# Kernel optimization log

Hardware: AMD Instinct MI355X
Metric: run time of the kernel (lower is better)

Reference implementation:

```python
import jax, jax.numpy as jnp
import numpy as np


def _block(x, a, b):
    # [..., W, H, D] -> [..., W//a, H//b, a, b, D]
    w, h, d = x.shape[-3:]
    x = jnp.reshape(x, x.shape[:-3] + (w // a, a, h // b, b, d))
    return jnp.moveaxis(x, -4, -3)


def _combine(x, bs):
    # [..., W, H, D] -> [..., W//bs, H//bs, bs*bs*D]
    x = _block(x, bs, bs)
    return jnp.reshape(x, x.shape[:-3] + (-1,))


def _normalize(x):
    x = x - jnp.mean(x, axis=-1, keepdims=True)
    return x / (jnp.linalg.norm(x, axis=-1, keepdims=True) + 1e-05)


def setup_inputs() -> dict:
    key = jax.random.key(0)
    k1, k2 = jax.random.split(key)
    x = jax.random.normal(k1, (8, 128, 128, 64), dtype=jnp.float32)
    y = jax.random.normal(k2, (8, 128, 128, 64), dtype=jnp.float32)
    return {"x": x, "y": y, "blocksize": 4}


def reference(x, y, blocksize):
    shape = x.shape
    xc = _normalize(_combine(x, blocksize))  # [B, W/bs, H/bs, F]
    yc = _normalize(_combine(y, blocksize))
    yf = jnp.reshape(yc, (-1, yc.shape[-1]))  # [M, F] codebook
    # single similarity matrix, reused for min-loss and argmax (original
    # computed jnp.inner twice -- same math)
    sim = jnp.einsum('...f,mf->...m', xc, yf)  # [B, W/bs, H/bs, M]
    cosloss = jnp.mean(jnp.min(1.0 - sim, axis=-1))
    idx = jnp.argmax(sim, axis=-1)
    # one-hot matmul against yf == top-1 gather (argmax picks first max, as
    # does the original I = (argmax - arange == 0) construction)
    new_x = jnp.take(yf, idx, axis=0)  # [B, W/bs, H/bs, F]
    new_x = jnp.reshape(new_x, new_x.shape[:-1] + (blocksize, blocksize, -1))
    new_x = jnp.swapaxes(new_x, -4, -3)
    new_x = jnp.reshape(new_x, shape)
    return cosloss, new_x
```

## Files before the change

kernel.cpp:

```cpp
#include <hip/hip_runtime.h>
#include <math.h>


#define NROWS 8192
#define KY 1024
#define NCH 32
#define EPS 3e-4f
#define FEPS 8e-4f

typedef _Float16 v8h __attribute__((ext_vector_type(8)));
typedef float f32x4 __attribute__((ext_vector_type(4)));

__device__ __forceinline__ void gload16(const _Float16* g, _Float16* l) {
    __builtin_amdgcn_global_load_lds(
        (const __attribute__((address_space(1))) void*)g,
        (__attribute__((address_space(3))) void*)l, 16, 0, 0);
}

__device__ __forceinline__ unsigned umax(unsigned a, unsigned b) { return a > b ? a : b; }
__device__ __forceinline__ unsigned umin(unsigned a, unsigned b) { return a < b ? a : b; }

__device__ __forceinline__ unsigned packKey(float v, int col) {
    unsigned b = __float_as_uint(v);
    b ^= (unsigned)((int)b >> 31) | 0x80000000u;
    return (b & 0xFFFFE000u) | (unsigned)(8191 - col);
}

__device__ __forceinline__ float unpackApprox(unsigned k) {
    unsigned kb = k & 0xFFFFE000u;
    unsigned b = (kb & 0x80000000u) ? (kb ^ 0x80000000u) : ~kb;
    return __uint_as_float(b);
}

#define KMERGE(a1, a2, a3, b1, b2, b3) do {                                 \
    unsigned _n1 = umax(a1, b1);                                            \
    unsigned _n2 = umax(umin(a1, b1), umax(a2, b2));                        \
    unsigned _n3 = umax(umax(a3, b3), umax(umin(a1, b2), umin(a2, b1)));    \
    a1 = _n1; a2 = _n2; a3 = _n3;                                           \
} while (0)

__global__ __launch_bounds__(256) void normSplitKernel(
    const float* __restrict__ x, const float* __restrict__ y,
    _Float16* __restrict__ Xh, _Float16* __restrict__ Xl,
    _Float16* __restrict__ Yh, _Float16* __restrict__ Yl,
    int* __restrict__ flagCnt) {
    if (blockIdx.x == 0 && threadIdx.x == 0) *flagCnt = 0;
    int gr = blockIdx.x * 4 + (threadIdx.x >> 6);
    int ln = threadIdx.x & 63;
    bool isX = gr < NROWS;
    int row = isX ? gr : gr - NROWS;
    const float* src = isX ? x : y;
    _Float16* dh = isX ? Xh : Yh;
    _Float16* dl = isX ? Xl : Yl;
    int b = row >> 10, wq = (row >> 5) & 31, hq = row & 31;
    int a = ln >> 4, c = (ln >> 2) & 3, d0 = (ln & 3) << 4;
    const float* p = &src[(((size_t)(b * 128) + wq * 4 + a) * 128 + hq * 4 + c) * 64 + d0];
    float vv[16];
    *(float4*)(vv + 0)  = *(const float4*)(p + 0);
    *(float4*)(vv + 4)  = *(const float4*)(p + 4);
    *(float4*)(vv + 8)  = *(const float4*)(p + 8);
    *(float4*)(vv + 12) = *(const float4*)(p + 12);
    double s = 0.0;
    #pragma unroll
    for (int q = 0; q < 16; q++) s += (double)vv[q];
    #pragma unroll
    for (int m = 1; m < 64; m <<= 1) s += __shfl_xor(s, m, 64);
    double mean = s * (1.0 / 1024.0);
    double ss = 0.0;
    #pragma unroll
    for (int q = 0; q < 16; q++) {
        double d = (double)vv[q] - mean;
        ss += d * d;
    }
    #pragma unroll
    for (int m = 1; m < 64; m <<= 1) ss += __shfl_xor(ss, m, 64);
    double scale = 1.0 / (sqrt(ss) + 1e-5);
    _Float16 hi[16], lo[16];
    #pragma unroll
    for (int q = 0; q < 16; q++) {
        float f = (float)(((double)vv[q] - mean) * scale);
        _Float16 h = (_Float16)f;
        hi[q] = h;
        lo[q] = (_Float16)(f - (float)h);
    }
    size_t f0 = (size_t)row * KY + (ln << 4);
    *(v8h*)&dh[f0]     = *(v8h*)(hi);
    *(v8h*)&dh[f0 + 8] = *(v8h*)(hi + 8);
    *(v8h*)&dl[f0]     = *(v8h*)(lo);
    *(v8h*)&dl[f0 + 8] = *(v8h*)(lo + 8);
}

__global__ __launch_bounds__(512, 2) void simKernel(
    const _Float16* __restrict__ Xh, const _Float16* __restrict__ Yh,
    float* __restrict__ pV1, unsigned* __restrict__ pK1,
    unsigned* __restrict__ pK2, unsigned* __restrict__ pK3) {
    __shared__ __align__(16) _Float16 As[2][2][128 * 64];
    __shared__ __align__(16) _Float16 Bs[2][2][128 * 64];
    __shared__ unsigned sK[2][4][128][3];
    __shared__ float sE[2][4][128];
    const int t = threadIdx.x;
    const int l = t & 63, w = t >> 6;
    const int wr = w >> 2, wc = w & 3;
    const int quad = l >> 4, lm = l & 15;
    const int flat = blockIdx.x;
    const int bx = flat >> 5, by = flat & 31;
    const int r0 = bx * 256, c0 = by * 256;

    f32x4 acc[8][4];
    #pragma unroll
    for (int i = 0; i < 8; i++)
        #pragma unroll
        for (int j = 0; j < 4; j++) acc[i][j] = (f32x4){0.f, 0.f, 0.f, 0.f};

    const int lh = l >> 3;
    const int scol = ((l & 7) ^ lh) << 3;
    const _Float16* gA = Xh + (size_t)(r0 + w * 8 + lh) * KY + scol;
    const _Float16* gB = Yh + (size_t)(c0 + w * 8 + lh) * KY + scol;
    const int w512 = w * 512;

#define STAGE_H(Ms, gM, bb, h, ktt) do {                                       \
    gload16(gM + (size_t)((h) * 128) * KY + (ktt) * 64,      &Ms[bb][h][w512]); \
    gload16(gM + (size_t)((h) * 128 + 64) * KY + (ktt) * 64, &Ms[bb][h][w512 + 4096]); \
} while (0)

    const int sw7 = lm & 7;
    const int cK0 = (quad ^ sw7) << 3;
    const int cK1 = ((4 + quad) ^ sw7) << 3;
    const int aOff = lm * 64;
    const int bSub = (wc & 1) * 4096 + lm * 64;

    STAGE_H(As, gA, 0, 0, 0); STAGE_H(As, gA, 0, 1, 0);
    STAGE_H(Bs, gB, 0, 0, 0); STAGE_H(Bs, gB, 0, 1, 0);
    asm volatile("s_waitcnt vmcnt(0)" ::: "memory");
    __builtin_amdgcn_s_barrier();

    #pragma unroll 1
    for (int kt = 0; kt < 16; kt++) {
        const int b = kt & 1, bn = b ^ 1;
        const int ktn = (kt + 1) & 15;
        const _Float16* Ah = &As[b][wr][0];
        const _Float16* Bh = &Bs[b][wc >> 1][0];
        v8h af[4], bf[4];

        #pragma unroll
        for (int i = 0; i < 4; i++) af[i] = *(const v8h*)&Ah[i * 1024 + aOff + cK0];
        #pragma unroll
        for (int j = 0; j < 4; j++) bf[j] = *(const v8h*)&Bh[bSub + j * 1024 + cK0];
        STAGE_H(As, gA, bn, 0, ktn);
        __builtin_amdgcn_s_barrier();
        asm volatile("s_waitcnt lgkmcnt(0)" ::: "memory");
        __builtin_amdgcn_sched_barrier(0);
        __builtin_amdgcn_s_setprio(1);
        #pragma unroll
        for (int j = 0; j < 4; j++)
            #pragma unroll
            for (int i = 0; i < 4; i++)
                acc[i][j] = __builtin_amdgcn_mfma_f32_16x16x32_f16(af[i], bf[j], acc[i][j], 0, 0, 0);
        __builtin_amdgcn_s_setprio(0);
        __builtin_amdgcn_s_barrier();

        #pragma unroll
        for (int i = 0; i < 4; i++) af[i] = *(const v8h*)&Ah[4096 + i * 1024 + aOff + cK0];
        STAGE_H(As, gA, bn, 1, ktn);
        __builtin_amdgcn_s_barrier();
        asm volatile("s_waitcnt lgkmcnt(0)" ::: "memory");
        __builtin_amdgcn_sched_barrier(0);
        __builtin_amdgcn_s_setprio(1);
        #pragma unroll
        for (int j = 0; j < 4; j++)
            #pragma unroll
            for (int i = 0; i < 4; i++)
                acc[4 + i][j] = __builtin_amdgcn_mfma_f32_16x16x32_f16(af[i], bf[j], acc[4 + i][j], 0, 0, 0);
        __builtin_amdgcn_s_setprio(0);
        __builtin_amdgcn_s_barrier();

        #pragma unroll
        for (int i = 0; i < 4; i++) af[i] = *(const v8h*)&Ah[i * 1024 + aOff + cK1];
        #pragma unroll
        for (int j = 0; j < 4; j++) bf[j] = *(const v8h*)&Bh[bSub + j * 1024 + cK1];
        STAGE_H(Bs, gB, bn, 0, ktn);
        __builtin_amdgcn_s_barrier();
        asm volatile("s_waitcnt lgkmcnt(0)" ::: "memory");
        __builtin_amdgcn_sched_barrier(0);
        __builtin_amdgcn_s_setprio(1);
        #pragma unroll
        for (int j = 0; j < 4; j++)
            #pragma unroll
            for (int i = 0; i < 4; i++)
                acc[i][j] = __builtin_amdgcn_mfma_f32_16x16x32_f16(af[i], bf[j], acc[i][j], 0, 0, 0);
        __builtin_amdgcn_s_setprio(0);
        __builtin_amdgcn_s_barrier();

        #pragma unroll
        for (int i = 0; i < 4; i++) af[i] = *(const v8h*)&Ah[4096 + i * 1024 + aOff + cK1];
        STAGE_H(Bs, gB, bn, 1, ktn);
        __builtin_amdgcn_s_barrier();
        asm volatile("s_waitcnt lgkmcnt(0)" ::: "memory");
        __builtin_amdgcn_sched_barrier(0);
        __builtin_amdgcn_s_setprio(1);
        #pragma unroll
        for (int j = 0; j < 4; j++)
            #pragma unroll
            for (int i = 0; i < 4; i++)
                acc[4 + i][j] = __builtin_amdgcn_mfma_f32_16x16x32_f16(af[i], bf[j], acc[4 + i][j], 0, 0, 0);
        __builtin_amdgcn_s_setprio(0);
        asm volatile("s_waitcnt vmcnt(0)" ::: "memory");
        __builtin_amdgcn_s_barrier();
    }
#undef STAGE_H

    const int cbase = c0 + wc * 64 + lm;
    #pragma unroll
    for (int i = 0; i < 8; i++) {
        #pragma unroll
        for (int r = 0; r < 4; r++) {
            float v0 = acc[i][0][r], v1 = acc[i][1][r];
            float v2 = acc[i][2][r], v3 = acc[i][3][r];
            unsigned k0 = packKey(v0, cbase);
            unsigned k1 = packKey(v1, cbase + 16);
            unsigned k2 = packKey(v2, cbase + 32);
            unsigned k3 = packKey(v3, cbase + 48);
            unsigned h1 = umax(k0, k1), l1 = umin(k0, k1);
            unsigned h2 = umax(k2, k3), l2 = umin(k2, k3);
            unsigned a1 = umax(h1, h2);
            unsigned a2 = umax(umin(h1, h2), umax(l1, l2));
            unsigned a3 = umax(umin(h1, l2), umin(l1, h2));
            float ev = fmaxf(fmaxf(v0, v1), fmaxf(v2, v3));
            #pragma unroll
            for (int m = 1; m < 16; m <<= 1) {
                unsigned b1 = (unsigned)__shfl_xor((int)a1, m, 64);
                unsigned b2 = (unsigned)__shfl_xor((int)a2, m, 64);
                unsigned b3 = (unsigned)__shfl_xor((int)a3, m, 64);
                float be = __shfl_xor(ev, m, 64);
                KMERGE(a1, a2, a3, b1, b2, b3);
                ev = fmaxf(ev, be);
            }
            if (lm == 0) {
                int rr = i * 16 + quad * 4 + r;
                sK[wr][wc][rr][0] = a1; sK[wr][wc][rr][1] = a2; sK[wr][wc][rr][2] = a3;
                sE[wr][wc][rr] = ev;
            }
        }
    }
    __syncthreads();
    if (t < 256) {
        const int mwr = t >> 7, ri = t & 127;
        unsigned a1 = sK[mwr][0][ri][0], a2 = sK[mwr][0][ri][1], a3 = sK[mwr][0][ri][2];
        float ev = sE[mwr][0][ri];
        #pragma unroll
        for (int q = 1; q < 4; q++) {
            unsigned b1 = sK[mwr][q][ri][0], b2 = sK[mwr][q][ri][1], b3 = sK[mwr][q][ri][2];
            KMERGE(a1, a2, a3, b1, b2, b3);
            ev = fmaxf(ev, sE[mwr][q][ri]);
        }
        size_t o = (size_t)by * NROWS + (r0 + t);
        pV1[o] = ev;
        pK1[o] = a1; pK2[o] = a2; pK3[o] = a3;
    }
}

__global__ __launch_bounds__(256) void reduceKernel(
    const float* __restrict__ pV1, const unsigned* __restrict__ pK1,
    const unsigned* __restrict__ pK2, const unsigned* __restrict__ pK3,
    int* __restrict__ bestIdx, int* __restrict__ flagRows,
    int* __restrict__ flagC2, int* __restrict__ flagC3,
    int* __restrict__ flagCnt, float* __restrict__ blkSum) {
    int t = threadIdx.x;
    int g = blockIdx.x * 256 + t;
    int row = g >> 2, sub = g & 3;
    unsigned a1 = 0, a2 = 0, a3 = 0;
    float ev = -1e30f;
    #pragma unroll
    for (int k = 0; k < 8; k++) {
        size_t o = (size_t)(sub + (k << 2)) * NROWS + row;
        unsigned b1 = pK1[o], b2 = pK2[o], b3 = pK3[o];
        float e = pV1[o];
        KMERGE(a1, a2, a3, b1, b2, b3);
        ev = fmaxf(ev, e);
    }
    #pragma unroll
    for (int m = 1; m < 4; m <<= 1) {
        unsigned b1 = (unsigned)__shfl_xor((int)a1, m, 64);
        unsigned b2 = (unsigned)__shfl_xor((int)a2, m, 64);
        unsigned b3 = (unsigned)__shfl_xor((int)a3, m, 64);
        float be = __shfl_xor(ev, m, 64);
        KMERGE(a1, a2, a3, b1, b2, b3);
        ev = fmaxf(ev, be);
    }
    bool lead = (t & 3) == 0;
    if (lead) {
        bestIdx[row] = 8191 - (int)(a1 & 8191u);
        if (ev - unpackApprox(a2) < FEPS) {
            int s = atomicAdd(flagCnt, 1);
            flagRows[s] = row;
            flagC2[s] = 8191 - (int)(a2 & 8191u);
            flagC3[s] = 8191 - (int)(a3 & 8191u);
        }
    }
    double sum = lead ? 1.0 - (double)ev : 0.0;
    __shared__ double sh[4];
    #pragma unroll
    for (int off = 32; off; off >>= 1) sum += __shfl_down(sum, off, 64);
    if ((t & 63) == 0) sh[t >> 6] = sum;
    __syncthreads();
    if (t == 0) blkSum[blockIdx.x] = (float)(sh[0] + sh[1] + sh[2] + sh[3]);
}

__global__ __launch_bounds__(256) void refineKernel(
    const _Float16* __restrict__ Xh, const _Float16* __restrict__ Xl,
    const _Float16* __restrict__ Yh, const _Float16* __restrict__ Yl,
    int* __restrict__ bestIdx, const int* __restrict__ flagRows,
    const int* __restrict__ flagC2, const int* __restrict__ flagC3,
    const int* __restrict__ flagCnt) {
    int n = *flagCnt;
    int wave = (blockIdx.x << 2) + (threadIdx.x >> 6);
    int ln = threadIdx.x & 63;
    for (int fi = wave; fi < n; fi += gridDim.x * 4) {
        int row = flagRows[fi];
        int cand[3];
        cand[0] = bestIdx[row]; cand[1] = flagC2[fi]; cand[2] = flagC3[fi];
        double d[3];
        #pragma unroll
        for (int c = 0; c < 3; c++) {
            double p = 0.0;
            int yr = cand[c];
            #pragma unroll
            for (int q = 0; q < 16; q++) {
                int k = (ln << 4) + q;
                float xv = (float)Xh[(size_t)row * KY + k] + (float)Xl[(size_t)row * KY + k];
                float yv = (float)Yh[(size_t)yr * KY + k] + (float)Yl[(size_t)yr * KY + k];
                p += (double)xv * yv;
            }
            #pragma unroll
            for (int m = 1; m < 64; m <<= 1) p += __shfl_xor(p, m, 64);
            d[c] = p;
        }
        if (ln == 0) {
            int bi = cand[0]; double bv = d[0];
            #pragma unroll
            for (int c = 1; c < 3; c++) {
                if (d[c] > bv || (d[c] == bv && cand[c] < bi)) { bv = d[c]; bi = cand[c]; }
            }
            bestIdx[row] = bi;
        }
    }
}

__global__ __launch_bounds__(256) void gatherKernel(
    const _Float16* __restrict__ Yh, const _Float16* __restrict__ Yl,
    const int* __restrict__ bestIdx, const float* __restrict__ blkSum,
    float* __restrict__ out) {
    int t = threadIdx.x;
    if (blockIdx.x == 0 && t == 0) {
        double s = 0.0;
        for (int i = 0; i < 128; i++) s += (double)blkSum[i];
        out[0] = (float)(s / 8192.0);
    }
    int g = (blockIdx.x * 256 + t) << 2;
    int b = g >> 20, wq = (g >> 13) & 127, hq = (g >> 6) & 127, d = g & 63;
    int row = (b << 10) + ((wq >> 2) << 5) + (hq >> 2);
    int f = ((wq & 3) << 8) + ((hq & 3) << 6) + d;
    size_t base = (size_t)bestIdx[row] * KY + f;
    const _Float16* ph = &Yh[base];
    const _Float16* pl = &Yl[base];
    out[1 + g + 0] = (float)ph[0] + (float)pl[0];
    out[1 + g + 1] = (float)ph[1] + (float)pl[1];
    out[1 + g + 2] = (float)ph[2] + (float)pl[2];
    out[1 + g + 3] = (float)ph[3] + (float)pl[3];
}

extern "C" void kernel_launch(void* const* d_in, const int* in_sizes, int n_in,
                              void* d_out, int out_size, void* d_ws, size_t ws_size,
                              hipStream_t stream) {
    const float* x = (const float*)d_in[0];
    const float* y = (const float*)d_in[1];
    float* out = (float*)d_out;
    char* ws = (char*)d_ws;
    _Float16* Xh  = (_Float16*)(ws);
    _Float16* Xl  = (_Float16*)(ws + 16777216u);
    _Float16* Yh  = (_Float16*)(ws + 33554432u);
    _Float16* Yl  = (_Float16*)(ws + 50331648u);
    float* pV1    = (float*)(ws + 67108864u);
    unsigned* pK1 = (unsigned*)(ws + 69206016u);
    unsigned* pK2 = (unsigned*)(ws + 71303168u);
    unsigned* pK3 = (unsigned*)(ws + 73400320u);
    int* bestIdx  = (int*)  (ws + 79691776u);
    int* flagRows = (int*)  (ws + 79724544u);
    int* flagC2   = (int*)  (ws + 79757312u);
    int* flagC3   = (int*)  (ws + 79790080u);
    int* flagCnt  = (int*)  (ws + 79822848u);
    float* blkSum = (float*)(ws + 79822976u);

    normSplitKernel<<<4096, 256, 0, stream>>>(x, y, Xh, Xl, Yh, Yl, flagCnt);
    simKernel<<<1024, 512, 0, stream>>>(Xh, Yh, pV1, pK1, pK2, pK3);
    reduceKernel<<<128, 256, 0, stream>>>(pV1, pK1, pK2, pK3,
                                          bestIdx, flagRows, flagC2, flagC3, flagCnt, blkSum);
    refineKernel<<<64, 256, 0, stream>>>(Xh, Xl, Yh, Yl, bestIdx,
                                         flagRows, flagC2, flagC3, flagCnt);
    gatherKernel<<<8192, 256, 0, stream>>>(Yh, Yl, bestIdx, blkSum, out);
}
```

Measured before the change: 320.3 us.

## Split LDS staging by K-half and wait only on the oldest loads

The shared-memory tiles are reorganized from row-half buffers (128 rows x 64 k) into K-half buffers (256 rows x 32 k), with a new 4-column XOR swizzle. Each phase now consumes a whole K-half of A and B, so the two halves are issued as separate load groups. Waits use vmcnt(4) instead of vmcnt(0), letting the second half's loads stay in flight while the first half is computed. This aims to hide global-to-LDS latency inside the K loop, at the cost of more fragile wait accounting and a different bank-conflict pattern.

```diff
diff --git a/kernel.cpp b/kernel.cpp
--- a/kernel.cpp
+++ b/kernel.cpp
@@ -94,8 +94,8 @@
     const _Float16* __restrict__ Xh, const _Float16* __restrict__ Yh,
     float* __restrict__ pV1, unsigned* __restrict__ pK1,
     unsigned* __restrict__ pK2, unsigned* __restrict__ pK3) {
-    __shared__ __align__(16) _Float16 As[2][2][128 * 64];
-    __shared__ __align__(16) _Float16 Bs[2][2][128 * 64];
+    __shared__ __align__(16) _Float16 As[2][2][256 * 32];
+    __shared__ __align__(16) _Float16 Bs[2][2][256 * 32];
     __shared__ unsigned sK[2][4][128][3];
     __shared__ float sE[2][4][128];
     const int t = threadIdx.x;
@@ -112,41 +112,39 @@
         #pragma unroll
         for (int j = 0; j < 4; j++) acc[i][j] = (f32x4){0.f, 0.f, 0.f, 0.f};
 
-    const int lh = l >> 3;
-    const int scol = ((l & 7) ^ lh) << 3;
-    const _Float16* gA = Xh + (size_t)(r0 + w * 8 + lh) * KY + scol;
-    const _Float16* gB = Yh + (size_t)(c0 + w * 8 + lh) * KY + scol;
+    const int lh4 = l >> 2;
+    const int sc = ((l & 3) ^ (lh4 & 3)) << 3;
+    const _Float16* gA = Xh + (size_t)(r0 + w * 16 + lh4) * KY + sc;
+    const _Float16* gB = Yh + (size_t)(c0 + w * 16 + lh4) * KY + sc;
     const int w512 = w * 512;
 
-#define STAGE_H(Ms, gM, bb, h, ktt) do {                                       \
-    gload16(gM + (size_t)((h) * 128) * KY + (ktt) * 64,      &Ms[bb][h][w512]); \
-    gload16(gM + (size_t)((h) * 128 + 64) * KY + (ktt) * 64, &Ms[bb][h][w512 + 4096]); \
+#define STG(Ms, gM, bb, kh, ktt) do {                                          \
+    gload16(gM + (ktt) * 64 + (kh) * 32,                    &Ms[bb][kh][w512]); \
+    gload16(gM + (size_t)128 * KY + (ktt) * 64 + (kh) * 32, &Ms[bb][kh][w512 + 4096]); \
 } while (0)
 
-    const int sw7 = lm & 7;
-    const int cK0 = (quad ^ sw7) << 3;
-    const int cK1 = ((4 + quad) ^ sw7) << 3;
-    const int aOff = lm * 64;
-    const int bSub = (wc & 1) * 4096 + lm * 64;
-
-    STAGE_H(As, gA, 0, 0, 0); STAGE_H(As, gA, 0, 1, 0);
-    STAGE_H(Bs, gB, 0, 0, 0); STAGE_H(Bs, gB, 0, 1, 0);
-    asm volatile("s_waitcnt vmcnt(0)" ::: "memory");
+    const int cswz = (quad ^ (lm & 3)) << 3;
+    const int aRow0 = (wr * 128 + lm) * 32;
+    const int bRow0 = (wc * 64 + lm) * 32;
+
+    STG(As, gA, 0, 0, 0);
+    STG(Bs, gB, 0, 0, 0);
+    STG(As, gA, 0, 1, 0);
+    STG(Bs, gB, 0, 1, 0);
+    asm volatile("s_waitcnt vmcnt(4)" ::: "memory");
     __builtin_amdgcn_s_barrier();
 
     #pragma unroll 1
     for (int kt = 0; kt < 16; kt++) {
         const int b = kt & 1, bn = b ^ 1;
         const int ktn = (kt + 1) & 15;
-        const _Float16* Ah = &As[b][wr][0];
-        const _Float16* Bh = &Bs[b][wc >> 1][0];
         v8h af[4], bf[4];
 
         #pragma unroll
-        for (int i = 0; i < 4; i++) af[i] = *(const v8h*)&Ah[i * 1024 + aOff + cK0];
-        #pragma unroll
-        for (int j = 0; j < 4; j++) bf[j] = *(const v8h*)&Bh[bSub + j * 1024 + cK0];
-        STAGE_H(As, gA, bn, 0, ktn);
+        for (int i = 0; i < 4; i++) af[i] = *(const v8h*)&As[b][0][aRow0 + i * 512 + cswz];
+        #pragma unroll
+        for (int j = 0; j < 4; j++) bf[j] = *(const v8h*)&Bs[b][0][bRow0 + j * 512 + cswz];
+        STG(As, gA, bn, 0, ktn);
         __builtin_amdgcn_s_barrier();
         asm volatile("s_waitcnt lgkmcnt(0)" ::: "memory");
         __builtin_amdgcn_sched_barrier(0);
@@ -160,8 +158,8 @@
         __builtin_amdgcn_s_barrier();
 
         #pragma unroll
-        for (int i = 0; i < 4; i++) af[i] = *(const v8h*)&Ah[4096 + i * 1024 + aOff + cK0];
-        STAGE_H(As, gA, bn, 1, ktn);
+        for (int i = 0; i < 4; i++) af[i] = *(const v8h*)&As[b][0][aRow0 + 2048 + i * 512 + cswz];
+        STG(Bs, gB, bn, 0, ktn);
         __builtin_amdgcn_s_barrier();
         asm volatile("s_waitcnt lgkmcnt(0)" ::: "memory");
         __builtin_amdgcn_sched_barrier(0);
@@ -172,13 +170,14 @@
             for (int i = 0; i < 4; i++)
                 acc[4 + i][j] = __builtin_amdgcn_mfma_f32_16x16x32_f16(af[i], bf[j], acc[4 + i][j], 0, 0, 0);
         __builtin_amdgcn_s_setprio(0);
-        __builtin_amdgcn_s_barrier();
-
-        #pragma unroll
-        for (int i = 0; i < 4; i++) af[i] = *(const v8h*)&Ah[i * 1024 + aOff + cK1];
-        #pragma unroll
-        for (int j = 0; j < 4; j++) bf[j] = *(const v8h*)&Bh[bSub + j * 1024 + cK1];
-        STAGE_H(Bs, gB, bn, 0, ktn);
+        asm volatile("s_waitcnt vmcnt(4)" ::: "memory");
+        __builtin_amdgcn_s_barrier();
+
+        #pragma unroll
+        for (int i = 0; i < 4; i++) af[i] = *(const v8h*)&As[b][1][aRow0 + i * 512 + cswz];
+        #pragma unroll
+        for (int j = 0; j < 4; j++) bf[j] = *(const v8h*)&Bs[b][1][bRow0 + j * 512 + cswz];
+        STG(As, gA, bn, 1, ktn);
         __builtin_amdgcn_s_barrier();
         asm volatile("s_waitcnt lgkmcnt(0)" ::: "memory");
         __builtin_amdgcn_sched_barrier(0);
@@ -192,8 +191,8 @@
         __builtin_amdgcn_s_barrier();
 
         #pragma unroll
-        for (int i = 0; i < 4; i++) af[i] = *(const v8h*)&Ah[4096 + i * 1024 + aOff + cK1];
-        STAGE_H(Bs, gB, bn, 1, ktn);
+        for (int i = 0; i < 4; i++) af[i] = *(const v8h*)&As[b][1][aRow0 + 2048 + i * 512 + cswz];
+        STG(Bs, gB, bn, 1, ktn);
         __builtin_amdgcn_s_barrier();
         asm volatile("s_waitcnt lgkmcnt(0)" ::: "memory");
         __builtin_amdgcn_sched_barrier(0);
@@ -204,10 +203,11 @@
             for (int i = 0; i < 4; i++)
                 acc[4 + i][j] = __builtin_amdgcn_mfma_f32_16x16x32_f16(af[i], bf[j], acc[4 + i][j], 0, 0, 0);
         __builtin_amdgcn_s_setprio(0);
-        asm volatile("s_waitcnt vmcnt(0)" ::: "memory");
-        __builtin_amdgcn_s_barrier();
-    }
-#undef STAGE_H
+        asm volatile("s_waitcnt vmcnt(4)" ::: "memory");
+        __builtin_amdgcn_s_barrier();
+    }
+#undef STG
+    asm volatile("s_waitcnt vmcnt(0)" ::: "memory");
 
     const int cbase = c0 + wc * 64 + lm;
     #pragma unroll
```

Measured after the change: 340.1 us. 1.06x slower.
